# Kernel tuning notes

Hardware: AMD Instinct MI355X
Metric: run time of the kernel (lower is better)

The kernel has to match this reference:

```python
import jax, jax.numpy as jnp
import numpy as np

B, S, D, H, V, C = 4, 2048, 1024, 16, 32000, 10
FFN_DIM = 2 * D
HD = D // H
SCALE = float(np.sqrt(HD))


def _posenc(seq, d):
    pos = jnp.arange(seq, dtype=jnp.float32)[:, None]
    div = jnp.exp(jnp.arange(0, d, 2, dtype=jnp.float32) * (-np.log(10000.0) / d))
    pe = jnp.zeros((seq, d), dtype=jnp.float32)
    pe = pe.at[:, 0::2].set(jnp.sin(pos * div))
    pe = pe.at[:, 1::2].set(jnp.cos(pos * div))
    return pe


def _layernorm(x, g, b, eps=1e-5):
    mu = jnp.mean(x, axis=-1, keepdims=True)
    var = jnp.mean(jnp.square(x - mu), axis=-1, keepdims=True)
    return (x - mu) * jax.lax.rsqrt(var + eps) * g + b


def setup_inputs() -> dict:
    key = jax.random.key(0)
    ks = jax.random.split(key, 10)
    x_ids = jax.random.randint(ks[0], (B, S), 0, V, dtype=jnp.int64 if jax.config.jax_enable_x64 else jnp.int32)
    mask = jnp.ones((B, S), dtype=jnp.int32)
    emb = (jax.random.normal(ks[1], (V, D), jnp.float32) * 0.02).at[0].set(0.0)  # padding_idx=0
    qkv_w = jax.random.normal(ks[2], (3 * D, D), jnp.float32) * 0.02
    fc_w = jax.random.normal(ks[3], (D, D), jnp.float32) * 0.02
    fc_b = jnp.zeros((D,), jnp.float32)
    ln1_g = jnp.ones((D,), jnp.float32); ln1_b = jnp.zeros((D,), jnp.float32)
    ffn_w1 = jax.random.normal(ks[4], (FFN_DIM, D), jnp.float32) * 0.02
    ffn_b1 = jnp.zeros((FFN_DIM,), jnp.float32)
    ffn_w2 = jax.random.normal(ks[5], (D, FFN_DIM), jnp.float32) * 0.02
    ffn_b2 = jnp.zeros((D,), jnp.float32)
    ln2_g = jnp.ones((D,), jnp.float32); ln2_b = jnp.zeros((D,), jnp.float32)
    pr_w1 = jax.random.normal(ks[6], (D, D), jnp.float32) * 0.02
    pr_b1 = jnp.zeros((D,), jnp.float32)
    pr_w2 = jax.random.normal(ks[7], (C, D), jnp.float32) * 0.02
    pr_b2 = jnp.zeros((C,), jnp.float32)
    return dict(x_ids=x_ids, mask=mask, emb=emb, qkv_w=qkv_w, fc_w=fc_w, fc_b=fc_b,
                ln1_g=ln1_g, ln1_b=ln1_b, ffn_w1=ffn_w1, ffn_b1=ffn_b1,
                ffn_w2=ffn_w2, ffn_b2=ffn_b2, ln2_g=ln2_g, ln2_b=ln2_b,
                pr_w1=pr_w1, pr_b1=pr_b1, pr_w2=pr_w2, pr_b2=pr_b2)


def reference(x_ids, mask, emb, qkv_w, fc_w, fc_b, ln1_g, ln1_b,
              ffn_w1, ffn_b1, ffn_w2, ffn_b2, ln2_g, ln2_b,
              pr_w1, pr_b1, pr_w2, pr_b2):
    # embedding + absolute positional encoding
    x = emb[x_ids] + _posenc(S, D)  # [B,S,D]
    residual = x
    # multi-head attention (dropout is identity at eval)
    qkv = jnp.einsum('bsd,ed->bse', x, qkv_w)  # [B,S,3D]
    q, k, v = jnp.split(qkv, 3, axis=-1)
    q = q.reshape(B, S, H, HD)
    k = k.reshape(B, S, H, HD)
    v = v.reshape(B, S, H, HD)
    attn = jnp.einsum('bqhd,bkhd->bhqk', q, k) / SCALE  # [B,H,S,S]
    attn = jnp.where(mask[:, None, None, :] == 0, -jnp.inf, attn)
    attn = jax.nn.softmax(attn, axis=-1)
    o = jnp.einsum('bhqk,bkhd->bqhd', attn, v).reshape(B, S, D)
    o = jnp.einsum('bsd,ed->bse', o, fc_w) + fc_b
    x = _layernorm(o + residual, ln1_g, ln1_b)
    # FFN block (residual + LayerNorm inside)
    h = jax.nn.gelu(jnp.einsum('bsd,fd->bsf', x, ffn_w1) + ffn_b1, approximate=False)
    h = jnp.einsum('bsf,df->bsd', h, ffn_w2) + ffn_b2
    x = _layernorm(h + x, ln2_g, ln2_b)
    # masked max-pool over sequence
    x = jnp.where(mask[:, :, None] == 0, -jnp.inf, x).max(axis=1)  # [B,D]
    # prediction head
    h = jax.nn.gelu(x @ pr_w1.T + pr_b1, approximate=False)
    logits = h @ pr_w2.T + pr_b2  # [B,C]
    return logits
```

## Files before the change

### kernel.cpp

```cpp
#include <hip/hip_runtime.h>
#include <math.h>

#define B_   4
#define S_   2048
#define D_   1024
#define H_   16
#define HD_  64
#define C_   10
#define FFN_ 2048
#define M_   (B_ * S_)
#define D3_  (3 * D_)

typedef unsigned short u16;
typedef __bf16 bf16x8 __attribute__((ext_vector_type(8)));
typedef float  f32x4  __attribute__((ext_vector_type(4)));

#define EXPSCL 0.18033688011112042f

__device__ __forceinline__ u16 f2bf(float f) {
  union { float f; unsigned u; } x; x.f = f;
  unsigned r = x.u + 0x7fffu + ((x.u >> 16) & 1u);
  return (u16)(r >> 16);
}
__device__ __forceinline__ unsigned cvtpk(float lo, float hi) {
  unsigned r;
  asm("v_cvt_pk_bf16_f32 %0, %1, %2" : "=v"(r) : "v"(lo), "v"(hi));
  return r;
}
__device__ __forceinline__ float gelu_f(float x) {
  return 0.5f * x * (1.f + erff(x * 0.70710678118654752440f));
}
__device__ __forceinline__ void gload_lds16(const void* g, void* l) {
  __builtin_amdgcn_global_load_lds(
      (const __attribute__((address_space(1))) unsigned int*)g,
      (__attribute__((address_space(3))) unsigned int*)l, 16, 0, 0);
}
__device__ __forceinline__ bf16x8 ldsfrag(const u16* buf, int rowbase, int fr, int kb) {
  return *(const bf16x8*)&buf[(rowbase + fr) * 64 + ((kb ^ (fr & 7)) << 3)];
}

#define CV0 786432
#define CV1 262144
#define CV2 524288
#define CV3 524288
__global__ __launch_bounds__(256) void cvt4_kernel(const float* __restrict__ s0,
                                                   const float* __restrict__ s1,
                                                   const float* __restrict__ s2,
                                                   const float* __restrict__ s3,
                                                   u16* __restrict__ d0,
                                                   u16* __restrict__ d1,
                                                   u16* __restrict__ d2,
                                                   u16* __restrict__ d3) {
  int v = blockIdx.x * 256 + threadIdx.x;
  const float* s; u16* d;
  if (v < CV0) { s = s0; d = d0; }
  else if (v < CV0 + CV1) { s = s1; d = d1; v -= CV0; }
  else if (v < CV0 + CV1 + CV2) { s = s2; d = d2; v -= CV0 + CV1; }
  else { s = s3; d = d3; v -= CV0 + CV1 + CV2; }
  const int i = v * 4;
  f32x4 x = *(const f32x4*)&s[i];
  ushort4 o;
  o.x = f2bf(x[0]); o.y = f2bf(x[1]); o.z = f2bf(x[2]); o.w = f2bf(x[3]);
  *(ushort4*)&d[i] = o;
}

__global__ __launch_bounds__(256) void embed_kernel(const int* __restrict__ ids,
                                                    const float* __restrict__ emb,
                                                    float* __restrict__ resid,
                                                    u16* __restrict__ xb) {
  const int m  = blockIdx.x;
  const int s  = m & (S_ - 1);
  const int id = ids[m];
  const int d0 = threadIdx.x * 4;
  const f32x4 e = *(const f32x4*)&emb[(size_t)id * D_ + d0];
  const float fs = (float)s;
  const float f0 = __expf((float)d0 * (-9.210340371976184f / 1024.0f));
  const float f1 = __expf((float)(d0 + 2) * (-9.210340371976184f / 1024.0f));
  float s0, c0, s1, c1;
  __sincosf(fs * f0, &s0, &c0);
  __sincosf(fs * f1, &s1, &c1);
  f32x4 v;
  v[0] = e[0] + s0; v[1] = e[1] + c0; v[2] = e[2] + s1; v[3] = e[3] + c1;
  *(f32x4*)&resid[(size_t)m * D_ + d0] = v;
  ushort4 pk;
  pk.x = f2bf(v[0]); pk.y = f2bf(v[1]); pk.z = f2bf(v[2]); pk.w = f2bf(v[3]);
  *(ushort4*)&xb[(size_t)m * D_ + d0] = pk;
}

template <int BIAS, int GELU, int OUTBF, int QSCALE>
__global__ __launch_bounds__(256) void gemm_bt(const u16* __restrict__ A,
                                               const u16* __restrict__ W,
                                               const float* __restrict__ bias,
                                               float* __restrict__ outf,
                                               u16* __restrict__ outb,
                                               int M, int N, int K) {
  __shared__ u16 As[128 * 64];
  __shared__ u16 Bs[128 * 64];
  const int tid  = threadIdx.x;
  const int lane = tid & 63;
  const int w    = tid >> 6;
  const int nx  = gridDim.x;
  const int nwg = nx * gridDim.y;
  int t = blockIdx.y * nx + blockIdx.x;
  t = (t & 7) * (nwg >> 3) + (t >> 3);
  const int bx = t % nx, by = t / nx;
  const int l3   = lane >> 3;
  const int sb   = (lane & 7) ^ l3;
  const u16* Ag0 = A + (size_t)(by * 128 + w * 32 + l3) * K + sb * 8;
  const u16* Wg0 = W + (size_t)(bx * 128 + w * 32 + l3) * K + sb * 8;

  f32x4 acc[4][4] = {};
  const int wr  = (w & 1) * 64;
  const int wc  = (w >> 1) * 64;
  const int fr  = lane & 15;
  const int fq  = lane >> 4;

  for (int kt = 0; kt < K; kt += 64) {
#pragma unroll
    for (int c = 0; c < 4; ++c) {
      gload_lds16(Ag0 + (size_t)(c * 8) * K + kt, &As[(w * 32 + c * 8) * 64]);
      gload_lds16(Wg0 + (size_t)(c * 8) * K + kt, &Bs[(w * 32 + c * 8) * 64]);
    }
    __syncthreads();
#pragma unroll
    for (int ks = 0; ks < 2; ++ks) {
      const int kb = ks * 4 + fq;
      bf16x8 af[4], bfr[4];
#pragma unroll
      for (int i = 0; i < 4; ++i) af[i] = ldsfrag(As, wr + i * 16, fr, kb);
#pragma unroll
      for (int j = 0; j < 4; ++j) bfr[j] = ldsfrag(Bs, wc + j * 16, fr, kb);
#pragma unroll
      for (int i = 0; i < 4; ++i)
#pragma unroll
        for (int j = 0; j < 4; ++j)
          acc[i][j] = __builtin_amdgcn_mfma_f32_16x16x32_bf16(bfr[j], af[i], acc[i][j], 0, 0, 0);
    }
    __syncthreads();
  }

  const float qs = (QSCALE && bx < 8) ? EXPSCL : 1.f;
#pragma unroll
  for (int i = 0; i < 4; ++i) {
    const int m = by * 128 + wr + i * 16 + fr;
#pragma unroll
    for (int j = 0; j < 4; ++j) {
      const int nb = bx * 128 + wc + j * 16 + fq * 4;
      f32x4 v = acc[i][j];
      if (BIAS) v += *(const f32x4*)&bias[nb];
      if (GELU) {
        v[0] = gelu_f(v[0]); v[1] = gelu_f(v[1]);
        v[2] = gelu_f(v[2]); v[3] = gelu_f(v[3]);
      }
      if (QSCALE) v *= qs;
      if (OUTBF) {
        ushort4 pk;
        pk.x = f2bf(v[0]); pk.y = f2bf(v[1]); pk.z = f2bf(v[2]); pk.w = f2bf(v[3]);
        *(ushort4*)&outb[(size_t)m * N + nb] = pk;
      } else {
        *(f32x4*)&outf[(size_t)m * N + nb] = v;
      }
    }
  }
}

__global__ __launch_bounds__(256) void vtrans_kernel(const u16* __restrict__ qkv,
                                                     u16* __restrict__ vt) {
  __shared__ u16 t[64 * 65];
  const int tid = threadIdx.x;
  const int st = blockIdx.x, h = blockIdx.y, b = blockIdx.z;
  {
    const int r = tid & 63, cg = tid >> 6;
    const u16* src = qkv + (size_t)(b * S_ + st * 64 + r) * D3_ + 2 * D_ + h * 64 + cg * 16;
    union { uint4 q; u16 s[8]; } a, c;
    a.q = *(const uint4*)src;
    c.q = *(const uint4*)(src + 8);
    u16* dl = &t[r * 65 + cg * 16];
#pragma unroll
    for (int k = 0; k < 8; ++k) { dl[k] = a.s[k]; dl[8 + k] = c.s[k]; }
  }
  __syncthreads();
  const int d = tid >> 2, sq = tid & 3;
  union { uint4 q[2]; u16 s[16]; } o;
#pragma unroll
  for (int k = 0; k < 16; ++k) o.s[k] = t[(sq * 16 + k) * 65 + d];
  u16* dst = vt + ((size_t)((b * H_ + h) * 64 + d)) * S_ + st * 64 + sq * 16;
  *(uint4*)dst = o.q[0];
  *(uint4*)(dst + 8) = o.q[1];
}

__global__ __launch_bounds__(256) void attn_mfma_kernel(const u16* __restrict__ qkv,
                                                        const u16* __restrict__ vt,
                                                        const int* __restrict__ mask,
                                                        u16* __restrict__ attno) {
  __shared__ u16 Ks[64 * 64];
  __shared__ u16 Vts[64 * 64];
  __shared__ u16 Ps[4][32 * 64];
  const int tid = threadIdx.x, lane = tid & 63, w = tid >> 6;
  int t = (blockIdx.z * 16 + blockIdx.y) * 16 + blockIdx.x;
  t = (t & 7) * 128 + (t >> 3);
  const int qt = t & 15, h = (t >> 4) & 15, b = t >> 8;
  const int l3 = lane >> 3;
  const int sb = (lane & 7) ^ l3;
  const int fr = lane & 15, fq = lane >> 4;
  u16* PsFlat = &Ps[0][0];

  {
    const u16* qbase = qkv + (size_t)(b * S_ + qt * 128 + w * 32) * D3_ + h * 64 + sb * 8;
#pragma unroll
    for (int c = 0; c < 4; ++c)
      gload_lds16(qbase + (size_t)(c * 8 + l3) * D3_, &PsFlat[(w * 32 + c * 8) * 64]);
  }

  bool ALLV;
  {
    const int4* mp = (const int4*)&mask[b * S_];
    int mv = 1;
#pragma unroll
    for (int tt = 0; tt < 8; ++tt) {
      const int4 m4 = mp[tt * 64 + lane];
      mv &= (m4.x != 0) & (m4.y != 0) & (m4.z != 0) & (m4.w != 0);
    }
    ALLV = (__ballot(mv != 0) == ~0ull);
  }

  __syncthreads();

  bf16x8 qf[2][2];
#pragma unroll
  for (int ks = 0; ks < 2; ++ks)
#pragma unroll
    for (int i = 0; i < 2; ++i)
      qf[ks][i] = ldsfrag(PsFlat, w * 32 + i * 16, fr, ks * 4 + fq);

  __syncthreads();

  float l_st[2] = {0.f, 0.f};
  f32x4 ot[4][2] = {};
  u16* PsW = Ps[w];

  for (int kt = 0; kt < S_ / 64; ++kt) {
    {
      const u16* kbase = qkv + (size_t)(b * S_ + kt * 64 + w * 16) * D3_ + D_ + h * 64 + sb * 8;
      gload_lds16(kbase + (size_t)l3 * D3_, &Ks[(w * 16) * 64]);
      gload_lds16(kbase + (size_t)(8 + l3) * D3_, &Ks[(w * 16 + 8) * 64]);
      const u16* vbase = vt + ((size_t)((b * H_ + h) * 64 + w * 16)) * S_ + kt * 64 + sb * 8;
      gload_lds16(vbase + (size_t)l3 * S_, &Vts[(w * 16) * 64]);
      gload_lds16(vbase + (size_t)(8 + l3) * S_, &Vts[(w * 16 + 8) * 64]);
    }
    __syncthreads();

    f32x4 sf[4][2] = {};
#pragma unroll
    for (int ks = 0; ks < 2; ++ks) {
      const int kb = ks * 4 + fq;
      __builtin_amdgcn_s_setprio(1);
#pragma unroll
      for (int r4 = 0; r4 < 4; ++r4) {
        bf16x8 kf = ldsfrag(Ks, r4 * 16, fr, kb);
        sf[r4][0] = __builtin_amdgcn_mfma_f32_16x16x32_bf16(kf, qf[ks][0], sf[r4][0], 0, 0, 0);
        sf[r4][1] = __builtin_amdgcn_mfma_f32_16x16x32_bf16(kf, qf[ks][1], sf[r4][1], 0, 0, 0);
      }
      __builtin_amdgcn_s_setprio(0);
    }
    if (!ALLV) {
#pragma unroll
      for (int r4 = 0; r4 < 4; ++r4) {
        const int4 mm = *(const int4*)&mask[b * S_ + kt * 64 + r4 * 16 + fq * 4];
        f32x4 vb;
        vb[0] = mm.x ? 0.f : -1e30f;
        vb[1] = mm.y ? 0.f : -1e30f;
        vb[2] = mm.z ? 0.f : -1e30f;
        vb[3] = mm.w ? 0.f : -1e30f;
        sf[r4][0] += vb;
        sf[r4][1] += vb;
      }
    }

#pragma unroll
    for (int i = 0; i < 2; ++i) {
      const int prow = i * 16 + fr;
      u16* pw = PsW + prow * 64;
      float sum = l_st[i];
#pragma unroll
      for (int r4 = 0; r4 < 4; ++r4) {
        const float p0 = __builtin_exp2f(sf[r4][i][0]);
        const float p1 = __builtin_exp2f(sf[r4][i][1]);
        const float p2 = __builtin_exp2f(sf[r4][i][2]);
        const float p3 = __builtin_exp2f(sf[r4][i][3]);
        sum += (p0 + p1) + (p2 + p3);
        const int bk0 = 2 * r4 + (fq >> 1);
        const int off = ((bk0 ^ (prow & 7)) << 3) + ((fq & 1) << 2);
        uint2 pk; pk.x = cvtpk(p0, p1); pk.y = cvtpk(p2, p3);
        *(uint2*)&pw[off] = pk;
      }
      l_st[i] = sum;
    }
    asm volatile("s_waitcnt lgkmcnt(0)" ::: "memory");

#pragma unroll
    for (int ks = 0; ks < 2; ++ks) {
      const int kb = ks * 4 + fq;
      bf16x8 pf0 = ldsfrag(PsW, 0, fr, kb);
      bf16x8 pf1 = ldsfrag(PsW, 16, fr, kb);
      __builtin_amdgcn_s_setprio(1);
#pragma unroll
      for (int db = 0; db < 4; ++db) {
        bf16x8 vf = ldsfrag(Vts, db * 16, fr, kb);
        ot[db][0] = __builtin_amdgcn_mfma_f32_16x16x32_bf16(vf, pf0, ot[db][0], 0, 0, 0);
        ot[db][1] = __builtin_amdgcn_mfma_f32_16x16x32_bf16(vf, pf1, ot[db][1], 0, 0, 0);
      }
      __builtin_amdgcn_s_setprio(0);
    }
    __syncthreads();
  }

#pragma unroll
  for (int i = 0; i < 2; ++i) {
    float l = l_st[i];
    l += __shfl_xor(l, 16);
    l += __shfl_xor(l, 32);
    const float inv = (l > 0.f) ? 1.f / l : 0.f;
    const int qrow = qt * 128 + w * 32 + i * 16 + fr;
    u16* dst = attno + (size_t)(b * S_ + qrow) * D_ + h * 64 + fq * 4;
#pragma unroll
    for (int db = 0; db < 4; ++db) {
      ushort4 pk;
      pk.x = f2bf(ot[db][i][0] * inv);
      pk.y = f2bf(ot[db][i][1] * inv);
      pk.z = f2bf(ot[db][i][2] * inv);
      pk.w = f2bf(ot[db][i][3] * inv);
      *(ushort4*)&dst[db * 16] = pk;
    }
  }
}

template <int WRITEB>
__global__ __launch_bounds__(256) void ln_kernel(const float* __restrict__ a,
                                                 const float* __restrict__ res,
                                                 const float* __restrict__ g,
                                                 const float* __restrict__ be,
                                                 float* __restrict__ outf,
                                                 u16* __restrict__ outb) {
  const int row = blockIdx.x, tid = threadIdx.x;
  const int lane = tid & 63, w = tid >> 6;
  const size_t base = (size_t)row * D_ + tid * 4;
  const f32x4 va = *(const f32x4*)(a + base);
  const f32x4 vr = *(const f32x4*)(res + base);
  const f32x4 v  = va + vr;
  float s = v[0] + v[1] + v[2] + v[3];
#pragma unroll
  for (int o = 32; o > 0; o >>= 1) s += __shfl_xor(s, o);
  __shared__ float red[8];
  if (lane == 0) red[w] = s;
  __syncthreads();
  const float mu = (red[0] + red[1] + red[2] + red[3]) * (1.f / D_);
  const f32x4 d = v - mu;
  float s2 = d[0] * d[0] + d[1] * d[1] + d[2] * d[2] + d[3] * d[3];
#pragma unroll
  for (int o = 32; o > 0; o >>= 1) s2 += __shfl_xor(s2, o);
  if (lane == 0) red[4 + w] = s2;
  __syncthreads();
  const float var = (red[4] + red[5] + red[6] + red[7]) * (1.f / D_);
  const float rs = rsqrtf(var + 1e-5f);
  f32x4 y;
#pragma unroll
  for (int k = 0; k < 4; ++k) {
    const int ch = tid * 4 + k;
    y[k] = d[k] * rs * g[ch] + be[ch];
  }
  *(f32x4*)&outf[base] = y;
  if (WRITEB) {
    ushort4 pk;
    pk.x = f2bf(y[0]); pk.y = f2bf(y[1]); pk.z = f2bf(y[2]); pk.w = f2bf(y[3]);
    *(ushort4*)&outb[base] = pk;
  }
}

__global__ __launch_bounds__(256) void pool_part_kernel(const float* __restrict__ x,
                                                        const int* __restrict__ mask,
                                                        float* __restrict__ part) {
  const int b = blockIdx.y, ch = blockIdx.x;
  const int d0 = threadIdx.x * 4;
  f32x4 acc = {-INFINITY, -INFINITY, -INFINITY, -INFINITY};
  for (int ss = 0; ss < 64; ++ss) {
    const int s = ch * 64 + ss;
    if (mask[b * S_ + s] != 0) {
      const f32x4 v = *(const f32x4*)&x[(size_t)(b * S_ + s) * D_ + d0];
      acc[0] = fmaxf(acc[0], v[0]);
      acc[1] = fmaxf(acc[1], v[1]);
      acc[2] = fmaxf(acc[2], v[2]);
      acc[3] = fmaxf(acc[3], v[3]);
    }
  }
  *(f32x4*)&part[(size_t)(b * 32 + ch) * D_ + d0] = acc;
}
__global__ __launch_bounds__(256) void pool_final_kernel(const float* __restrict__ part,
                                                         float* __restrict__ pooled) {
  const int b = blockIdx.x;
  const int d0 = threadIdx.x * 4;
  f32x4 acc = {-INFINITY, -INFINITY, -INFINITY, -INFINITY};
  for (int ch = 0; ch < 32; ++ch) {
    const f32x4 v = *(const f32x4*)&part[(size_t)(b * 32 + ch) * D_ + d0];
    acc[0] = fmaxf(acc[0], v[0]);
    acc[1] = fmaxf(acc[1], v[1]);
    acc[2] = fmaxf(acc[2], v[2]);
    acc[3] = fmaxf(acc[3], v[3]);
  }
  *(f32x4*)&pooled[(size_t)b * D_ + d0] = acc;
}

__global__ __launch_bounds__(256) void head1_kernel(const float* __restrict__ pooled,
                                                    const float* __restrict__ w,
                                                    const float* __restrict__ bias,
                                                    float* __restrict__ hh) {
  const int lane = threadIdx.x & 63;
  const int gw = blockIdx.x * 4 + (threadIdx.x >> 6);
  const int b = gw >> 10, n = gw & 1023;
  const float* p  = pooled + b * 1024;
  const float* wr = w + (size_t)n * 1024;
  float s = 0.f;
  for (int d = lane; d < 1024; d += 64) s += p[d] * wr[d];
#pragma unroll
  for (int off = 32; off > 0; off >>= 1) s += __shfl_xor(s, off);
  if (lane == 0) hh[b * 1024 + n] = gelu_f(s + bias[n]);
}
__global__ __launch_bounds__(256) void head2_kernel(const float* __restrict__ hh,
                                                    const float* __restrict__ w,
                                                    const float* __restrict__ bias,
                                                    float* __restrict__ out) {
  const int lane = threadIdx.x & 63;
  const int gw = blockIdx.x * 4 + (threadIdx.x >> 6);
  const int b = gw / 10, c = gw % 10;
  const float* p  = hh + b * 1024;
  const float* wr = w + (size_t)c * 1024;
  float s = 0.f;
  for (int d = lane; d < 1024; d += 64) s += p[d] * wr[d];
#pragma unroll
  for (int off = 32; off > 0; off >>= 1) s += __shfl_xor(s, off);
  if (lane == 0) out[b * 10 + c] = s + bias[c];
}

#define OFF_RESID  0UL
#define OFF_F1     33554432UL
#define OFF_XB     67108864UL
#define OFF_QKVB   83886080UL
#define OFF_ATTNO  134217728UL
#define OFF_WQKV   150994944UL
#define OFF_WFC    157286400UL
#define OFF_WF1    159383552UL
#define OFF_WF2    163577856UL
#define OFF_PART   167772160UL
#define OFF_POOLED 168296448UL
#define OFF_HH     168312832UL

extern "C" void kernel_launch(void* const* d_in, const int* in_sizes, int n_in,
                              void* d_out, int out_size, void* d_ws, size_t ws_size,
                              hipStream_t stream) {
  const int*   x_ids  = (const int*)d_in[0];
  const int*   mask   = (const int*)d_in[1];
  const float* emb    = (const float*)d_in[2];
  const float* qkv_w  = (const float*)d_in[3];
  const float* fc_w   = (const float*)d_in[4];
  const float* fc_b   = (const float*)d_in[5];
  const float* ln1_g  = (const float*)d_in[6];
  const float* ln1_b  = (const float*)d_in[7];
  const float* ffn_w1 = (const float*)d_in[8];
  const float* ffn_b1 = (const float*)d_in[9];
  const float* ffn_w2 = (const float*)d_in[10];
  const float* ffn_b2 = (const float*)d_in[11];
  const float* ln2_g  = (const float*)d_in[12];
  const float* ln2_b  = (const float*)d_in[13];
  const float* pr_w1  = (const float*)d_in[14];
  const float* pr_b1  = (const float*)d_in[15];
  const float* pr_w2  = (const float*)d_in[16];
  const float* pr_b2  = (const float*)d_in[17];
  float* out = (float*)d_out;
  char* ws = (char*)d_ws;

  float* resid  = (float*)(ws + OFF_RESID);
  float* f1     = (float*)(ws + OFF_F1);
  u16*   vtb    = (u16*)(ws + OFF_F1);
  u16*   xb     = (u16*)(ws + OFF_XB);
  u16*   qkvb   = (u16*)(ws + OFF_QKVB);
  u16*   hb     = (u16*)(ws + OFF_QKVB);
  u16*   attnob = (u16*)(ws + OFF_ATTNO);
  u16*   wqkvb  = (u16*)(ws + OFF_WQKV);
  u16*   wfcb   = (u16*)(ws + OFF_WFC);
  u16*   wf1b   = (u16*)(ws + OFF_WF1);
  u16*   wf2b   = (u16*)(ws + OFF_WF2);
  float* part   = (float*)(ws + OFF_PART);
  float* pooled = (float*)(ws + OFF_POOLED);
  float* hh     = (float*)(ws + OFF_HH);

  cvt4_kernel<<<8192, 256, 0, stream>>>(qkv_w, fc_w, ffn_w1, ffn_w2,
                                        wqkvb, wfcb, wf1b, wf2b);

  embed_kernel<<<M_, 256, 0, stream>>>(x_ids, emb, resid, xb);

  gemm_bt<0, 0, 1, 1><<<dim3(D3_ / 128, M_ / 128), 256, 0, stream>>>(
      xb, wqkvb, nullptr, nullptr, qkvb, M_, D3_, D_);

  vtrans_kernel<<<dim3(S_ / 64, H_, B_), 256, 0, stream>>>(qkvb, vtb);

  attn_mfma_kernel<<<dim3(S_ / 128, H_, B_), 256, 0, stream>>>(qkvb, vtb, mask, attnob);

  gemm_bt<1, 0, 0, 0><<<dim3(D_ / 128, M_ / 128), 256, 0, stream>>>(
      attnob, wfcb, fc_b, f1, nullptr, M_, D_, D_);

  ln_kernel<1><<<M_, 256, 0, stream>>>(f1, resid, ln1_g, ln1_b, resid, xb);

  gemm_bt<1, 1, 1, 0><<<dim3(FFN_ / 128, M_ / 128), 256, 0, stream>>>(
      xb, wf1b, ffn_b1, nullptr, hb, M_, FFN_, D_);

  gemm_bt<1, 0, 0, 0><<<dim3(D_ / 128, M_ / 128), 256, 0, stream>>>(
      hb, wf2b, ffn_b2, f1, nullptr, M_, D_, FFN_);

  ln_kernel<0><<<M_, 256, 0, stream>>>(f1, resid, ln2_g, ln2_b, f1, nullptr);

  pool_part_kernel<<<dim3(32, B_), 256, 0, stream>>>(f1, mask, part);
  pool_final_kernel<<<B_, 256, 0, stream>>>(part, pooled);

  head1_kernel<<<1024, 256, 0, stream>>>(pooled, pr_w1, pr_b1, hh);
  head2_kernel<<<10, 256, 0, stream>>>(hh, pr_w2, pr_b2, out);
}
```

Baseline: 605.1 us.

## Fuse prep kernels, write V transposed from QKV GEMM, MFMA row sums

Merges the weight conversion and embedding kernels into one launch. The QKV GEMM epilogue now writes the V part directly in transposed layout, which removes the separate transpose kernel. The attention softmax denominator is now computed by an extra MFMA against a vector of ones instead of scalar adds and shuffles. The transposed V stores are scattered 2-byte writes, which may be poorly coalesced.

```diff
diff --git a/kernel.cpp b/kernel.cpp
--- a/kernel.cpp
+++ b/kernel.cpp
@@ -43,56 +43,58 @@
 #define CV1 262144
 #define CV2 524288
 #define CV3 524288
-__global__ __launch_bounds__(256) void cvt4_kernel(const float* __restrict__ s0,
+__global__ __launch_bounds__(256) void prep_kernel(const float* __restrict__ s0,
                                                    const float* __restrict__ s1,
                                                    const float* __restrict__ s2,
                                                    const float* __restrict__ s3,
                                                    u16* __restrict__ d0,
                                                    u16* __restrict__ d1,
                                                    u16* __restrict__ d2,
-                                                   u16* __restrict__ d3) {
-  int v = blockIdx.x * 256 + threadIdx.x;
-  const float* s; u16* d;
-  if (v < CV0) { s = s0; d = d0; }
-  else if (v < CV0 + CV1) { s = s1; d = d1; v -= CV0; }
-  else if (v < CV0 + CV1 + CV2) { s = s2; d = d2; v -= CV0 + CV1; }
-  else { s = s3; d = d3; v -= CV0 + CV1 + CV2; }
-  const int i = v * 4;
-  f32x4 x = *(const f32x4*)&s[i];
-  ushort4 o;
-  o.x = f2bf(x[0]); o.y = f2bf(x[1]); o.z = f2bf(x[2]); o.w = f2bf(x[3]);
-  *(ushort4*)&d[i] = o;
-}
-
-__global__ __launch_bounds__(256) void embed_kernel(const int* __restrict__ ids,
-                                                    const float* __restrict__ emb,
-                                                    float* __restrict__ resid,
-                                                    u16* __restrict__ xb) {
-  const int m  = blockIdx.x;
-  const int s  = m & (S_ - 1);
-  const int id = ids[m];
-  const int d0 = threadIdx.x * 4;
-  const f32x4 e = *(const f32x4*)&emb[(size_t)id * D_ + d0];
-  const float fs = (float)s;
-  const float f0 = __expf((float)d0 * (-9.210340371976184f / 1024.0f));
-  const float f1 = __expf((float)(d0 + 2) * (-9.210340371976184f / 1024.0f));
-  float s0, c0, s1, c1;
-  __sincosf(fs * f0, &s0, &c0);
-  __sincosf(fs * f1, &s1, &c1);
-  f32x4 v;
-  v[0] = e[0] + s0; v[1] = e[1] + c0; v[2] = e[2] + s1; v[3] = e[3] + c1;
-  *(f32x4*)&resid[(size_t)m * D_ + d0] = v;
-  ushort4 pk;
-  pk.x = f2bf(v[0]); pk.y = f2bf(v[1]); pk.z = f2bf(v[2]); pk.w = f2bf(v[3]);
-  *(ushort4*)&xb[(size_t)m * D_ + d0] = pk;
-}
-
-template <int BIAS, int GELU, int OUTBF, int QSCALE>
+                                                   u16* __restrict__ d3,
+                                                   const int* __restrict__ ids,
+                                                   const float* __restrict__ emb,
+                                                   float* __restrict__ resid,
+                                                   u16* __restrict__ xb) {
+  if (blockIdx.x < 8192) {
+    int v = blockIdx.x * 256 + threadIdx.x;
+    const float* s; u16* d;
+    if (v < CV0) { s = s0; d = d0; }
+    else if (v < CV0 + CV1) { s = s1; d = d1; v -= CV0; }
+    else if (v < CV0 + CV1 + CV2) { s = s2; d = d2; v -= CV0 + CV1; }
+    else { s = s3; d = d3; v -= CV0 + CV1 + CV2; }
+    const int i = v * 4;
+    f32x4 x = *(const f32x4*)&s[i];
+    ushort4 o;
+    o.x = f2bf(x[0]); o.y = f2bf(x[1]); o.z = f2bf(x[2]); o.w = f2bf(x[3]);
+    *(ushort4*)&d[i] = o;
+  } else {
+    const int m  = blockIdx.x - 8192;
+    const int s  = m & (S_ - 1);
+    const int id = ids[m];
+    const int d4 = threadIdx.x * 4;
+    const f32x4 e = *(const f32x4*)&emb[(size_t)id * D_ + d4];
+    const float fs = (float)s;
+    const float f0 = __expf((float)d4 * (-9.210340371976184f / 1024.0f));
+    const float f1 = __expf((float)(d4 + 2) * (-9.210340371976184f / 1024.0f));
+    float s0v, c0v, s1v, c1v;
+    __sincosf(fs * f0, &s0v, &c0v);
+    __sincosf(fs * f1, &s1v, &c1v);
+    f32x4 v;
+    v[0] = e[0] + s0v; v[1] = e[1] + c0v; v[2] = e[2] + s1v; v[3] = e[3] + c1v;
+    *(f32x4*)&resid[(size_t)m * D_ + d4] = v;
+    ushort4 pk;
+    pk.x = f2bf(v[0]); pk.y = f2bf(v[1]); pk.z = f2bf(v[2]); pk.w = f2bf(v[3]);
+    *(ushort4*)&xb[(size_t)m * D_ + d4] = pk;
+  }
+}
+
+template <int BIAS, int GELU, int OUTBF, int QSCALE, int VSPLIT>
 __global__ __launch_bounds__(256) void gemm_bt(const u16* __restrict__ A,
                                                const u16* __restrict__ W,
                                                const float* __restrict__ bias,
                                                float* __restrict__ outf,
                                                u16* __restrict__ outb,
+                                               u16* __restrict__ vtout,
                                                int M, int N, int K) {
   __shared__ u16 As[128 * 64];
   __shared__ u16 Bs[128 * 64];
@@ -153,7 +155,16 @@
         v[2] = gelu_f(v[2]); v[3] = gelu_f(v[3]);
       }
       if (QSCALE) v *= qs;
-      if (OUTBF) {
+      if (VSPLIT && bx >= 16) {
+        const int hh = (nb - 2 * D_) >> 6;
+        const int dl = (nb - 2 * D_) & 63;
+        const int bb = m >> 11, ss = m & (S_ - 1);
+        u16* vdst = vtout + ((size_t)((bb * H_ + hh) * 64 + dl)) * S_ + ss;
+        vdst[0]          = f2bf(v[0]);
+        vdst[(size_t)S_]     = f2bf(v[1]);
+        vdst[(size_t)2 * S_] = f2bf(v[2]);
+        vdst[(size_t)3 * S_] = f2bf(v[3]);
+      } else if (OUTBF) {
         ushort4 pk;
         pk.x = f2bf(v[0]); pk.y = f2bf(v[1]); pk.z = f2bf(v[2]); pk.w = f2bf(v[3]);
         *(ushort4*)&outb[(size_t)m * N + nb] = pk;
@@ -162,31 +173,6 @@
       }
     }
   }
-}
-
-__global__ __launch_bounds__(256) void vtrans_kernel(const u16* __restrict__ qkv,
-                                                     u16* __restrict__ vt) {
-  __shared__ u16 t[64 * 65];
-  const int tid = threadIdx.x;
-  const int st = blockIdx.x, h = blockIdx.y, b = blockIdx.z;
-  {
-    const int r = tid & 63, cg = tid >> 6;
-    const u16* src = qkv + (size_t)(b * S_ + st * 64 + r) * D3_ + 2 * D_ + h * 64 + cg * 16;
-    union { uint4 q; u16 s[8]; } a, c;
-    a.q = *(const uint4*)src;
-    c.q = *(const uint4*)(src + 8);
-    u16* dl = &t[r * 65 + cg * 16];
-#pragma unroll
-    for (int k = 0; k < 8; ++k) { dl[k] = a.s[k]; dl[8 + k] = c.s[k]; }
-  }
-  __syncthreads();
-  const int d = tid >> 2, sq = tid & 3;
-  union { uint4 q[2]; u16 s[16]; } o;
-#pragma unroll
-  for (int k = 0; k < 16; ++k) o.s[k] = t[(sq * 16 + k) * 65 + d];
-  u16* dst = vt + ((size_t)((b * H_ + h) * 64 + d)) * S_ + st * 64 + sq * 16;
-  *(uint4*)dst = o.q[0];
-  *(uint4*)(dst + 8) = o.q[1];
 }
 
 __global__ __launch_bounds__(256) void attn_mfma_kernel(const u16* __restrict__ qkv,
@@ -235,8 +221,12 @@
 
   __syncthreads();
 
-  float l_st[2] = {0.f, 0.f};
+  bf16x8 onesf;
+#pragma unroll
+  for (int k = 0; k < 8; ++k) onesf[k] = (__bf16)1.0f;
+
   f32x4 ot[4][2] = {};
+  f32x4 otl[2] = {};
   u16* PsW = Ps[w];
 
   for (int kt = 0; kt < S_ / 64; ++kt) {
@@ -281,20 +271,17 @@
     for (int i = 0; i < 2; ++i) {
       const int prow = i * 16 + fr;
       u16* pw = PsW + prow * 64;
-      float sum = l_st[i];
 #pragma unroll
       for (int r4 = 0; r4 < 4; ++r4) {
         const float p0 = __builtin_exp2f(sf[r4][i][0]);
         const float p1 = __builtin_exp2f(sf[r4][i][1]);
         const float p2 = __builtin_exp2f(sf[r4][i][2]);
         const float p3 = __builtin_exp2f(sf[r4][i][3]);
-        sum += (p0 + p1) + (p2 + p3);
         const int bk0 = 2 * r4 + (fq >> 1);
         const int off = ((bk0 ^ (prow & 7)) << 3) + ((fq & 1) << 2);
         uint2 pk; pk.x = cvtpk(p0, p1); pk.y = cvtpk(p2, p3);
         *(uint2*)&pw[off] = pk;
       }
-      l_st[i] = sum;
     }
     asm volatile("s_waitcnt lgkmcnt(0)" ::: "memory");
 
@@ -310,6 +297,8 @@
         ot[db][0] = __builtin_amdgcn_mfma_f32_16x16x32_bf16(vf, pf0, ot[db][0], 0, 0, 0);
         ot[db][1] = __builtin_amdgcn_mfma_f32_16x16x32_bf16(vf, pf1, ot[db][1], 0, 0, 0);
       }
+      otl[0] = __builtin_amdgcn_mfma_f32_16x16x32_bf16(onesf, pf0, otl[0], 0, 0, 0);
+      otl[1] = __builtin_amdgcn_mfma_f32_16x16x32_bf16(onesf, pf1, otl[1], 0, 0, 0);
       __builtin_amdgcn_s_setprio(0);
     }
     __syncthreads();
@@ -317,9 +306,7 @@
 
 #pragma unroll
   for (int i = 0; i < 2; ++i) {
-    float l = l_st[i];
-    l += __shfl_xor(l, 16);
-    l += __shfl_xor(l, 32);
+    const float l = otl[i][0];
     const float inv = (l > 0.f) ? 1.f / l : 0.f;
     const int qrow = qt * 128 + w * 32 + i * 16 + fr;
     u16* dst = attno + (size_t)(b * S_ + qrow) * D_ + h * 64 + fq * 4;
@@ -493,28 +480,25 @@
   float* pooled = (float*)(ws + OFF_POOLED);
   float* hh     = (float*)(ws + OFF_HH);
 
-  cvt4_kernel<<<8192, 256, 0, stream>>>(qkv_w, fc_w, ffn_w1, ffn_w2,
-                                        wqkvb, wfcb, wf1b, wf2b);
-
-  embed_kernel<<<M_, 256, 0, stream>>>(x_ids, emb, resid, xb);
-
-  gemm_bt<0, 0, 1, 1><<<dim3(D3_ / 128, M_ / 128), 256, 0, stream>>>(
-      xb, wqkvb, nullptr, nullptr, qkvb, M_, D3_, D_);
-
-  vtrans_kernel<<<dim3(S_ / 64, H_, B_), 256, 0, stream>>>(qkvb, vtb);
+  prep_kernel<<<16384, 256, 0, stream>>>(qkv_w, fc_w, ffn_w1, ffn_w2,
+                                         wqkvb, wfcb, wf1b, wf2b,
+                                         x_ids, emb, resid, xb);
+
+  gemm_bt<0, 0, 1, 1, 1><<<dim3(D3_ / 128, M_ / 128), 256, 0, stream>>>(
+      xb, wqkvb, nullptr, nullptr, qkvb, vtb, M_, D3_, D_);
 
   attn_mfma_kernel<<<dim3(S_ / 128, H_, B_), 256, 0, stream>>>(qkvb, vtb, mask, attnob);
 
-  gemm_bt<1, 0, 0, 0><<<dim3(D_ / 128, M_ / 128), 256, 0, stream>>>(
-      attnob, wfcb, fc_b, f1, nullptr, M_, D_, D_);
+  gemm_bt<1, 0, 0, 0, 0><<<dim3(D_ / 128, M_ / 128), 256, 0, stream>>>(
+      attnob, wfcb, fc_b, f1, nullptr, nullptr, M_, D_, D_);
 
   ln_kernel<1><<<M_, 256, 0, stream>>>(f1, resid, ln1_g, ln1_b, resid, xb);
 
-  gemm_bt<1, 1, 1, 0><<<dim3(FFN_ / 128, M_ / 128), 256, 0, stream>>>(
-      xb, wf1b, ffn_b1, nullptr, hb, M_, FFN_, D_);
-
-  gemm_bt<1, 0, 0, 0><<<dim3(D_ / 128, M_ / 128), 256, 0, stream>>>(
-      hb, wf2b, ffn_b2, f1, nullptr, M_, D_, FFN_);
+  gemm_bt<1, 1, 1, 0, 0><<<dim3(FFN_ / 128, M_ / 128), 256, 0, stream>>>(
+      xb, wf1b, ffn_b1, nullptr, hb, nullptr, M_, FFN_, D_);
+
+  gemm_bt<1, 0, 0, 0, 0><<<dim3(D_ / 128, M_ / 128), 256, 0, stream>>>(
+      hb, wf2b, ffn_b2, f1, nullptr, nullptr, M_, D_, FFN_);
 
   ln_kernel<0><<<M_, 256, 0, stream>>>(f1, resid, ln2_g, ln2_b, f1, nullptr);
 
```

New measurement: 591.2 us. -2.3%, faster.
